# Kernel tuning notes

Hardware: AMD Instinct MI355X
Metric: run time of the kernel (lower is better)

## Reference

```python
import jax, jax.numpy as jnp
import numpy as np

N, E, K, F, R = 100000, 200000, 16, 32, 2
EPS = 1e-5

def setup_inputs() -> dict:
    key = jax.random.key(0)
    ks = jax.random.split(key, 32)
    inp = {}
    inp['x'] = jax.random.normal(ks[0], (N, F), jnp.float32)
    inp['y'] = jax.random.normal(ks[1], (E, F), jnp.float32)
    inp['deg_g'] = jax.random.uniform(ks[2], (N, 1), jnp.float32)
    inp['deg_lg'] = jax.random.uniform(ks[3], (E, 1), jnp.float32)
    inp['t_g'] = jax.random.randint(ks[4], (N, K), 0, N)
    inp['tt_g'] = jax.random.randint(ks[5], (N, K), 0, N)
    inp['t_lg'] = jax.random.randint(ks[6], (E, K), 0, E)
    inp['tt_lg'] = jax.random.randint(ks[7], (E, K), 0, E)
    inp['dst'] = jax.random.randint(ks[8], (E,), 0, N)
    inp['pm_pd'] = jax.random.randint(ks[9], (E,), 0, N)
    i = [10]
    def mk(shape):
        a = jax.random.normal(ks[i[0]], shape, jnp.float32) * 0.1
        i[0] += 1
        return a
    for nm in ['theta_x', 'theta_deg', 'theta_y', 'gamma_y', 'gamma_deg', 'gamma_x']:
        inp[nm + '_w'] = mk((F, F)); inp[nm + '_b'] = mk((F,))
    inp['theta_r_w'] = mk((R, F, F)); inp['theta_r_b'] = mk((R, F))
    inp['gamma_r_w'] = mk((R, F, F)); inp['gamma_r_b'] = mk((R, F))
    inp['bn_x_w'] = jnp.ones((F,), jnp.float32); inp['bn_x_b'] = jnp.zeros((F,), jnp.float32)
    inp['bn_y_w'] = jnp.ones((F,), jnp.float32); inp['bn_y_b'] = jnp.zeros((F,), jnp.float32)
    return inp

def _lin(a, w, b):
    return a @ w + b

def _bn(a, w, b):
    # BatchNorm1d in training mode: biased batch stats
    m = a.mean(axis=0)
    v = a.var(axis=0)
    return (a - m) / jnp.sqrt(v + EPS) * w + b

def _aggregate(z, t, tt):
    # per-node gather+sum over neighbor index lists (t: radius-0, tt: radius-1)
    return jnp.stack([z[t].sum(axis=1), z[tt].sum(axis=1)])  # [R, M, F]

def reference(x, y, deg_g, deg_lg, t_g, tt_g, t_lg, tt_lg, dst, pm_pd,
              theta_x_w, theta_x_b, theta_deg_w, theta_deg_b, theta_y_w, theta_y_b,
              gamma_y_w, gamma_y_b, gamma_deg_w, gamma_deg_b, gamma_x_w, gamma_x_b,
              theta_r_w, theta_r_b, gamma_r_w, gamma_r_b,
              bn_x_w, bn_x_b, bn_y_w, bn_y_b):
    n = F // 2
    pmpd_x = x[pm_pd]                                   # [E, F] embedding gather
    zs = _aggregate(x, t_g, tt_g)                        # [R, N, F]
    sum_x = jnp.einsum('rnf,rfo->no', zs, theta_r_w) + theta_r_b.sum(axis=0)
    pmpd_y = jax.ops.segment_sum(y, dst, num_segments=x.shape[0])  # copy_edge + sum
    xo = (_lin(x, theta_x_w, theta_x_b)
          + _lin(deg_g * x, theta_deg_w, theta_deg_b)
          + sum_x
          + _lin(pmpd_y, theta_y_w, theta_y_b))
    xo = jnp.concatenate([xo[:, :n], jax.nn.relu(xo[:, n:])], axis=1)
    xo = _bn(xo, bn_x_w, bn_x_b)
    zy = _aggregate(y, t_lg, tt_lg)                      # [R, E, F]
    sum_y = jnp.einsum('ref,rfo->eo', zy, gamma_r_w) + gamma_r_b.sum(axis=0)
    yo = (_lin(y, gamma_y_w, gamma_y_b)
          + _lin(deg_lg * y, gamma_deg_w, gamma_deg_b)
          + sum_y
          + _lin(pmpd_x, gamma_x_w, gamma_x_b))
    yo = jnp.concatenate([yo[:, :n], jax.nn.relu(yo[:, n:])], axis=1)
    yo = _bn(yo, bn_y_w, bn_y_b)
    return xo, yo
```

## Files before the change

kernel.cpp:

```cpp
#include <hip/hip_runtime.h>

#define NN 100000
#define NE 200000
#define MT (NN + NE)

typedef unsigned short u16;
typedef __attribute__((ext_vector_type(8))) short bf16x8;
typedef __attribute__((ext_vector_type(4))) float f32x4;

__device__ __forceinline__ float bf2f(u16 u) {
    union { unsigned int i; float f; } v; v.i = ((unsigned int)u) << 16; return v.f;
}
__device__ __forceinline__ u16 f2bf(float f) {
    union { unsigned int i; float f; } v; v.f = f;
    unsigned int r = v.i + 0x7fffu + ((v.i >> 16) & 1u);
    return (u16)(r >> 16);
}
__device__ __forceinline__ void unpack2(unsigned int u, float& lo, float& hi) {
    union { unsigned int i; float f; } a, b;
    a.i = u << 16; b.i = u & 0xffff0000u;
    lo = a.f; hi = b.f;
}
__device__ __forceinline__ unsigned int pack2(float a, float b) {
    return (unsigned int)f2bf(a) | ((unsigned int)f2bf(b) << 16);
}
__device__ __forceinline__ float loadf(const void* p, size_t i, int f32) {
    return f32 ? ((const float*)p)[i] : bf2f(((const u16*)p)[i]);
}
__device__ __forceinline__ void acc8(float a[8], uint4 g) {
    float e0, e1, e2, e3, e4, e5, e6, e7;
    unpack2(g.x, e0, e1); unpack2(g.y, e2, e3);
    unpack2(g.z, e4, e5); unpack2(g.w, e6, e7);
    a[0] += e0; a[1] += e1; a[2] += e2; a[3] += e3;
    a[4] += e4; a[5] += e5; a[6] += e6; a[7] += e7;
}

__global__ void detect_kernel(const unsigned int* __restrict__ x, int* flag) {
    __shared__ int cnt;
    if (threadIdx.x == 0) cnt = 0;
    __syncthreads();
    int bad = 0;
    for (int i = threadIdx.x; i < 1024; i += 256) {
        unsigned int e = (x[i] >> 7) & 0xFF;
        if (e == 0xFF || (e > 0 && (e < 107 || e > 134))) bad++;
    }
    atomicAdd(&cnt, bad);
    __syncthreads();
    if (threadIdx.x == 0) *flag = (cnt > 256) ? 1 : 0;
}

__global__ __launch_bounds__(256) void prep_kernel(
    const void* txw, const void* tdw, const void* tyw,
    const void* gyw, const void* gdw, const void* gxw,
    const void* trw, const void* grw,
    const void* txb, const void* tdb, const void* tyb,
    const void* gyb, const void* gdb, const void* gxb,
    const void* trb, const void* grb,
    u16* Bfx, u16* Bfy, float* bx, float* by, const int* flagp)
{
    int f32 = *flagp;
    int t = blockIdx.x * 256 + threadIdx.x;
    if (t < 4096) {
        int b = t >> 9, lane = (t >> 3) & 63, j = t & 7;
        int m = b >> 1;
        int k = ((lane >> 4) << 3) + j;
        int f = ((b & 1) << 4) + (lane & 15);
        size_t idx = (size_t)k * 32 + f;
        float v = (m == 0) ? loadf(txw, idx, f32) : (m == 1) ? loadf(tdw, idx, f32)
                : (m == 2) ? loadf(trw, idx, f32) : loadf(trw, 1024 + idx, f32);
        Bfx[t] = f2bf(v);
    } else if (t < 10240) {
        int e = t - 4096;
        int b = e >> 9, lane = (e >> 3) & 63, j = e & 7;
        int m = b >> 1;
        int k = ((lane >> 4) << 3) + j;
        int f = ((b & 1) << 4) + (lane & 15);
        size_t idx = (size_t)k * 32 + f;
        float v = (m == 0) ? loadf(gyw, idx, f32) : (m == 1) ? loadf(gdw, idx, f32)
                : (m == 2) ? loadf(grw, idx, f32) : (m == 3) ? loadf(grw, 1024 + idx, f32)
                : (m == 4) ? loadf(gxw, idx, f32) : loadf(tyw, idx, f32);
        Bfy[e] = f2bf(v);
    } else if (t < 10304) {
        int f = t - 10240;
        if (f < 32) {
            bx[f] = loadf(txb, f, f32) + loadf(tdb, f, f32) + loadf(tyb, f, f32)
                  + loadf(trb, f, f32) + loadf(trb, 32 + f, f32);
        } else {
            f -= 32;
            by[f] = loadf(gyb, f, f32) + loadf(gdb, f, f32) + loadf(gxb, f, f32)
                  + loadf(grb, f, f32) + loadf(grb, 32 + f, f32);
        }
    }
}

__global__ __launch_bounds__(256) void convert_kernel(
    const void* __restrict__ x, const void* __restrict__ y,
    u16* __restrict__ xb, u16* __restrict__ yb, const int* __restrict__ flagp)
{
    int f32 = *flagp;
    int t = blockIdx.x * 256 + threadIdx.x;
    if (t < NN * 4) {
        int r = t >> 2, q = t & 3;
        uint4 o;
        if (f32) {
            const float4* fp = (const float4*)((const float*)x + (size_t)r * 32 + q * 8);
            float4 v0 = fp[0], v1 = fp[1];
            o.x = pack2(v0.x, v0.y); o.y = pack2(v0.z, v0.w);
            o.z = pack2(v1.x, v1.y); o.w = pack2(v1.z, v1.w);
        } else {
            o = *(const uint4*)((const u16*)x + (size_t)r * 32 + q * 8);
        }
        *(uint4*)(xb + (size_t)r * 32 + q * 8) = o;
    } else if (t < MT * 4) {
        int t2 = t - NN * 4;
        int r = t2 >> 2, q = t2 & 3;
        uint4 o;
        if (f32) {
            const float4* fp = (const float4*)((const float*)y + (size_t)r * 32 + q * 8);
            float4 v0 = fp[0], v1 = fp[1];
            o.x = pack2(v0.x, v0.y); o.y = pack2(v0.z, v0.w);
            o.z = pack2(v1.x, v1.y); o.w = pack2(v1.z, v1.w);
        } else {
            o = *(const uint4*)((const u16*)y + (size_t)r * 32 + q * 8);
        }
        *(uint4*)(yb + (size_t)r * 32 + q * 8) = o;
    }
}

template<int IS_Y>
__global__ __launch_bounds__(256, 3) void fused_side(
    const u16* __restrict__ xb, const u16* __restrict__ yb,
    float* xacc,
    const u16* __restrict__ Bf, const float* __restrict__ bias,
    const void* __restrict__ deg,
    const int* __restrict__ tl, const int* __restrict__ ttl,
    const int* __restrict__ pm_pd, const int* __restrict__ dst,
    float* xpre, u16* __restrict__ ypre,
    float* __restrict__ stats, const int* __restrict__ flagp)
{
    __shared__ int s_t[1024];
    __shared__ int s_tt[1024];
    __shared__ float s_sum[32];
    __shared__ float s_sq[32];
    const int M = IS_Y ? NE : NN;
    int f32 = *flagp;
    int row0 = (int)blockIdx.x * 64;
    if (threadIdx.x < 32) { s_sum[threadIdx.x] = 0.f; s_sq[threadIdx.x] = 0.f; }
    int lim = (M - row0) * 16;
    for (int i = threadIdx.x; i < 1024; i += 256) {
        s_t[i]  = (i < lim) ? tl[(size_t)row0 * 16 + i]  : 0;
        s_tt[i] = (i < lim) ? ttl[(size_t)row0 * 16 + i] : 0;
    }
    __syncthreads();
    int lane = threadIdx.x & 63, wib = threadIdx.x >> 6;
    int r0 = row0 + wib * 16;
    if (r0 + 16 <= M) {
        const u16* tab = IS_Y ? yb : xb;
        int m = lane & 15, q = lane >> 4;
        int gr = r0 + m;
        const int* il  = &s_t[(wib * 16 + m) * 16];
        const int* ill = &s_tt[(wib * 16 + m) * 16];

        bf16x8 selfv = *(const bf16x8*)(tab + (size_t)gr * 32 + q * 8);
        union { u16 s[8]; bf16x8 v; } pm;
        if (IS_Y) {
            int ai = pm_pd[gr];
            pm.v = *(const bf16x8*)(xb + (size_t)ai * 32 + q * 8);
        }

        float aT[8]  = {0.f, 0.f, 0.f, 0.f, 0.f, 0.f, 0.f, 0.f};
        float aTT[8] = {0.f, 0.f, 0.f, 0.f, 0.f, 0.f, 0.f, 0.f};
        uint4 ga[8], gb[8];
#pragma unroll
        for (int j = 0; j < 8; ++j)
            ga[j] = *(const uint4*)(tab + (size_t)il[j] * 32 + q * 8);
#pragma unroll
        for (int j = 0; j < 8; ++j)
            gb[j] = *(const uint4*)(tab + (size_t)il[8 + j] * 32 + q * 8);
#pragma unroll
        for (int j = 0; j < 8; ++j) acc8(aT, ga[j]);
#pragma unroll
        for (int j = 0; j < 8; ++j)
            ga[j] = *(const uint4*)(tab + (size_t)ill[j] * 32 + q * 8);
#pragma unroll
        for (int j = 0; j < 8; ++j) acc8(aT, gb[j]);
#pragma unroll
        for (int j = 0; j < 8; ++j)
            gb[j] = *(const uint4*)(tab + (size_t)ill[8 + j] * 32 + q * 8);
#pragma unroll
        for (int j = 0; j < 8; ++j) acc8(aTT, ga[j]);
#pragma unroll
        for (int j = 0; j < 8; ++j) acc8(aTT, gb[j]);

        union { u16 s[8]; bf16x8 v; } ft, ftt;
#pragma unroll
        for (int j = 0; j < 8; ++j) { ft.s[j] = f2bf(aT[j]); ftt.s[j] = f2bf(aTT[j]); }

        const u16* bp = Bf + lane * 8;
#define BFR(b) (*(const bf16x8*)(bp + (b) * 512))
        f32x4 z = {0.f, 0.f, 0.f, 0.f};
        f32x4 a0, a1, d0, d1, c0 = z, c1 = z;
        a0 = __builtin_amdgcn_mfma_f32_16x16x32_bf16(selfv, BFR(0), z, 0, 0, 0);
        a1 = __builtin_amdgcn_mfma_f32_16x16x32_bf16(selfv, BFR(1), z, 0, 0, 0);
        d0 = __builtin_amdgcn_mfma_f32_16x16x32_bf16(selfv, BFR(2), z, 0, 0, 0);
        d1 = __builtin_amdgcn_mfma_f32_16x16x32_bf16(selfv, BFR(3), z, 0, 0, 0);
        a0 = __builtin_amdgcn_mfma_f32_16x16x32_bf16(ft.v,  BFR(4), a0, 0, 0, 0);
        a1 = __builtin_amdgcn_mfma_f32_16x16x32_bf16(ft.v,  BFR(5), a1, 0, 0, 0);
        a0 = __builtin_amdgcn_mfma_f32_16x16x32_bf16(ftt.v, BFR(6), a0, 0, 0, 0);
        a1 = __builtin_amdgcn_mfma_f32_16x16x32_bf16(ftt.v, BFR(7), a1, 0, 0, 0);
        if (IS_Y) {
            a0 = __builtin_amdgcn_mfma_f32_16x16x32_bf16(pm.v,  BFR(8),  a0, 0, 0, 0);
            a1 = __builtin_amdgcn_mfma_f32_16x16x32_bf16(pm.v,  BFR(9),  a1, 0, 0, 0);
            c0 = __builtin_amdgcn_mfma_f32_16x16x32_bf16(selfv, BFR(10), z, 0, 0, 0);
            c1 = __builtin_amdgcn_mfma_f32_16x16x32_bf16(selfv, BFR(11), z, 0, 0, 0);
        }
#undef BFR

        int n = m;
        int rowb = r0 + q * 4;
        float bl_ = bias[n], bh_ = bias[16 + n];
        float s0 = 0.f, q0 = 0.f, s1 = 0.f, q1 = 0.f;
#pragma unroll
        for (int i = 0; i < 4; ++i) {
            float dgi = loadf(deg, rowb + i, f32);
            size_t ro = (size_t)(rowb + i) * 32;
            float lo = a0[i] + dgi * d0[i] + bl_;
            float hi = a1[i] + dgi * d1[i] + bh_;
            if (!IS_Y) {
                lo += xacc[ro + n];
                hi += xacc[ro + 16 + n];
            }
            hi = fmaxf(hi, 0.f);
            if (!IS_Y) {
                xpre[ro + n]      = lo;
                xpre[ro + 16 + n] = hi;
            } else {
                ypre[ro + n]      = f2bf(lo);
                ypre[ro + 16 + n] = f2bf(hi);
                int d = dst[rowb + i];
                float* p = xacc + (size_t)d * 32;
                atomicAdd(p + n,      c0[i]);
                atomicAdd(p + 16 + n, c1[i]);
            }
            s0 += lo; q0 += lo * lo;
            s1 += hi; q1 += hi * hi;
        }
        atomicAdd(&s_sum[n], s0);      atomicAdd(&s_sq[n], q0);
        atomicAdd(&s_sum[16 + n], s1); atomicAdd(&s_sq[16 + n], q1);
    }
    __syncthreads();
    if (threadIdx.x < 32) {
        float* ss = stats + (IS_Y ? 64 : 0);
        atomicAdd(&ss[threadIdx.x], s_sum[threadIdx.x]);
        atomicAdd(&ss[32 + threadIdx.x], s_sq[threadIdx.x]);
    }
}

__global__ void finalize_stats(
    const float* stats,
    const void* bnxw, const void* bnxb, const void* bnyw, const void* bnyb,
    float* scsh, const int* flagp)
{
    int f32 = *flagp;
    int f = threadIdx.x;
    if (f < 32) {
        float m = stats[f] / (float)NN;
        float var = stats[32 + f] / (float)NN - m * m;
        float inv = rsqrtf(var + 1e-5f);
        float sc = loadf(bnxw, f, f32) * inv;
        scsh[f] = sc; scsh[32 + f] = loadf(bnxb, f, f32) - m * sc;
    } else if (f < 64) {
        int g = f - 32;
        float m = stats[64 + g] / (float)NE;
        float var = stats[96 + g] / (float)NE - m * m;
        float inv = rsqrtf(var + 1e-5f);
        float sc = loadf(bnyw, g, f32) * inv;
        scsh[64 + g] = sc; scsh[96 + g] = loadf(bnyb, g, f32) - m * sc;
    }
}

__global__ __launch_bounds__(256) void apply_bn(
    const float* __restrict__ xpre, const u16* __restrict__ ypre,
    const float* __restrict__ scsh, void* __restrict__ out,
    const int* __restrict__ flagp)
{
    int f32 = *flagp;
    int tid = blockIdx.x * 256 + threadIdx.x;
    if (tid >= MT * 8) return;
    int fq = (tid & 7) * 4;
    const float* sc;
    float4 v;
    if (tid < NN * 8) {
        v = ((const float4*)xpre)[tid];
        sc = scsh;
    } else {
        size_t off = (size_t)tid * 4 - (size_t)NN * 32;
        ushort4 u = *(const ushort4*)(ypre + off);
        v.x = bf2f(u.x); v.y = bf2f(u.y); v.z = bf2f(u.z); v.w = bf2f(u.w);
        sc = scsh + 64;
    }
    float o0 = v.x * sc[fq + 0] + sc[32 + fq + 0];
    float o1 = v.y * sc[fq + 1] + sc[32 + fq + 1];
    float o2 = v.z * sc[fq + 2] + sc[32 + fq + 2];
    float o3 = v.w * sc[fq + 3] + sc[32 + fq + 3];
    if (f32) {
        float4 o; o.x = o0; o.y = o1; o.z = o2; o.w = o3;
        ((float4*)out)[tid] = o;
    } else {
        ushort4 o; o.x = f2bf(o0); o.y = f2bf(o1); o.z = f2bf(o2); o.w = f2bf(o3);
        ((ushort4*)out)[tid] = o;
    }
}

extern "C" void kernel_launch(void* const* d_in, const int* in_sizes, int n_in,
                              void* d_out, int out_size, void* d_ws, size_t ws_size,
                              hipStream_t stream)
{
    const void* x      = d_in[0];
    const void* y      = d_in[1];
    const void* deg_g  = d_in[2];
    const void* deg_lg = d_in[3];
    const int* t_g   = (const int*)d_in[4];
    const int* tt_g  = (const int*)d_in[5];
    const int* t_lg  = (const int*)d_in[6];
    const int* tt_lg = (const int*)d_in[7];
    const int* dst   = (const int*)d_in[8];
    const int* pm_pd = (const int*)d_in[9];

    char* ws = (char*)d_ws;
    int*   flag = (int*)ws;
    u16* Bfx   = (u16*)(ws + 256);
    u16* Bfy   = Bfx + 4096;
    float* bx  = (float*)(ws + 24576);
    float* by  = bx + 32;
    float* stats = by + 32;
    float* scsh  = stats + 128;
    u16* xb    = (u16*)(ws + 65536);
    u16* yb    = xb + (size_t)NN * 32;
    float* xacc = (float*)(yb + (size_t)NE * 32);
    u16* ypre  = (u16*)(xacc + (size_t)NN * 32);

    hipMemsetAsync(stats, 0, 256 * sizeof(float), stream);
    hipMemsetAsync(xacc, 0, (size_t)NN * 32 * sizeof(float), stream);

    detect_kernel<<<1, 256, 0, stream>>>((const unsigned int*)x, flag);
    prep_kernel<<<41, 256, 0, stream>>>(
        d_in[10], d_in[12], d_in[14], d_in[16], d_in[18], d_in[20],
        d_in[22], d_in[24],
        d_in[11], d_in[13], d_in[15], d_in[17], d_in[19], d_in[21],
        d_in[23], d_in[25],
        Bfx, Bfy, bx, by, flag);
    convert_kernel<<<4688, 256, 0, stream>>>(x, y, xb, yb, flag);
    fused_side<1><<<3125, 256, 0, stream>>>(xb, yb, xacc, Bfy, by, deg_lg,
                                            t_lg, tt_lg, pm_pd, dst,
                                            (float*)0, ypre, stats, flag);
    fused_side<0><<<1563, 256, 0, stream>>>(xb, yb, xacc, Bfx, bx, deg_g,
                                            t_g, tt_g, pm_pd, dst,
                                            xacc , (u16*)0,
                                            stats, flag);
    finalize_stats<<<1, 64, 0, stream>>>(stats, d_in[26], d_in[27], d_in[28],
                                         d_in[29], scsh, flag);
    apply_bn<<<9375, 256, 0, stream>>>(xacc, ypre, scsh, d_out, flag);
}
```

Baseline: 405.5 us.

## Merge x and y side kernels into one interleaved launch with separate x-stats pass

```diff
diff --git a/kernel.cpp b/kernel.cpp
--- a/kernel.cpp
+++ b/kernel.cpp
@@ -128,28 +128,25 @@
 }
 
 template<int IS_Y>
-__global__ __launch_bounds__(256, 3) void fused_side(
+__device__ __forceinline__ void fused_body(
     const u16* __restrict__ xb, const u16* __restrict__ yb,
     float* xacc,
     const u16* __restrict__ Bf, const float* __restrict__ bias,
     const void* __restrict__ deg,
     const int* __restrict__ tl, const int* __restrict__ ttl,
     const int* __restrict__ pm_pd, const int* __restrict__ dst,
-    float* xpre, u16* __restrict__ ypre,
-    float* __restrict__ stats, const int* __restrict__ flagp)
-{
-    __shared__ int s_t[1024];
-    __shared__ int s_tt[1024];
-    __shared__ float s_sum[32];
-    __shared__ float s_sq[32];
+    float* __restrict__ xmfma, u16* __restrict__ ypre,
+    float* __restrict__ ystats, int f32, int sb,
+    int* s_t, int* s_tt, float* s_sum, float* s_sq)
+{
     const int M = IS_Y ? NE : NN;
-    int f32 = *flagp;
-    int row0 = (int)blockIdx.x * 64;
-    if (threadIdx.x < 32) { s_sum[threadIdx.x] = 0.f; s_sq[threadIdx.x] = 0.f; }
+    int row0 = sb * 64;
+    if (row0 >= M) return;
+    if (IS_Y && threadIdx.x < 32) { s_sum[threadIdx.x] = 0.f; s_sq[threadIdx.x] = 0.f; }
     int lim = (M - row0) * 16;
     for (int i = threadIdx.x; i < 1024; i += 256) {
-        s_t[i]  = (i < lim) ? tl[(size_t)row0 * 16 + i]  : 0;
-        s_tt[i] = (i < lim) ? ttl[(size_t)row0 * 16 + i] : 0;
+        s_t[i]  = (i < lim) ? __builtin_nontemporal_load(&tl[(size_t)row0 * 16 + i])  : 0;
+        s_tt[i] = (i < lim) ? __builtin_nontemporal_load(&ttl[(size_t)row0 * 16 + i]) : 0;
     }
     __syncthreads();
     int lane = threadIdx.x & 63, wib = threadIdx.x >> 6;
@@ -227,32 +224,90 @@
             float lo = a0[i] + dgi * d0[i] + bl_;
             float hi = a1[i] + dgi * d1[i] + bh_;
             if (!IS_Y) {
-                lo += xacc[ro + n];
-                hi += xacc[ro + 16 + n];
-            }
-            hi = fmaxf(hi, 0.f);
-            if (!IS_Y) {
-                xpre[ro + n]      = lo;
-                xpre[ro + 16 + n] = hi;
+                __builtin_nontemporal_store(lo, &xmfma[ro + n]);
+                __builtin_nontemporal_store(hi, &xmfma[ro + 16 + n]);
             } else {
-                ypre[ro + n]      = f2bf(lo);
-                ypre[ro + 16 + n] = f2bf(hi);
+                hi = fmaxf(hi, 0.f);
+                __builtin_nontemporal_store(f2bf(lo), &ypre[ro + n]);
+                __builtin_nontemporal_store(f2bf(hi), &ypre[ro + 16 + n]);
                 int d = dst[rowb + i];
                 float* p = xacc + (size_t)d * 32;
                 atomicAdd(p + n,      c0[i]);
                 atomicAdd(p + 16 + n, c1[i]);
+                s0 += lo; q0 += lo * lo;
+                s1 += hi; q1 += hi * hi;
             }
-            s0 += lo; q0 += lo * lo;
-            s1 += hi; q1 += hi * hi;
-        }
-        atomicAdd(&s_sum[n], s0);      atomicAdd(&s_sq[n], q0);
-        atomicAdd(&s_sum[16 + n], s1); atomicAdd(&s_sq[16 + n], q1);
-    }
+        }
+        if (IS_Y) {
+            atomicAdd(&s_sum[n], s0);      atomicAdd(&s_sq[n], q0);
+            atomicAdd(&s_sum[16 + n], s1); atomicAdd(&s_sq[16 + n], q1);
+        }
+    }
+    if (IS_Y) {
+        __syncthreads();
+        if (threadIdx.x < 32) {
+            atomicAdd(&ystats[threadIdx.x], s_sum[threadIdx.x]);
+            atomicAdd(&ystats[32 + threadIdx.x], s_sq[threadIdx.x]);
+        }
+    }
+}
+
+__global__ __launch_bounds__(256, 3) void fused_both(
+    const u16* __restrict__ xb, const u16* __restrict__ yb, float* xacc,
+    const u16* __restrict__ Bfx, const u16* __restrict__ Bfy,
+    const float* __restrict__ bx, const float* __restrict__ by,
+    const void* __restrict__ deg_g, const void* __restrict__ deg_lg,
+    const int* __restrict__ t_g, const int* __restrict__ tt_g,
+    const int* __restrict__ t_lg, const int* __restrict__ tt_lg,
+    const int* __restrict__ pm_pd, const int* __restrict__ dst,
+    float* __restrict__ xmfma, u16* __restrict__ ypre,
+    float* __restrict__ stats, const int* __restrict__ flagp)
+{
+    __shared__ int s_t[1024];
+    __shared__ int s_tt[1024];
+    __shared__ float s_sum[32];
+    __shared__ float s_sq[32];
+    int f32 = *flagp;
+    int bid = blockIdx.x;
+    int s = bid % 3;
+    if (s == 2) {
+        fused_body<0>(xb, yb, xacc, Bfx, bx, deg_g, t_g, tt_g, pm_pd, dst,
+                      xmfma, ypre, stats, f32, bid / 3,
+                      s_t, s_tt, s_sum, s_sq);
+    } else {
+        fused_body<1>(xb, yb, xacc, Bfy, by, deg_lg, t_lg, tt_lg, pm_pd, dst,
+                      xmfma, ypre, stats + 64, f32, (bid / 3) * 2 + s,
+                      s_t, s_tt, s_sum, s_sq);
+    }
+}
+
+__global__ __launch_bounds__(256) void xstats_kernel(
+    const float* __restrict__ xmfma, float* __restrict__ xacc,
+    float* __restrict__ stats)
+{
+    __shared__ float s_sum[32];
+    __shared__ float s_sq[32];
+    if (threadIdx.x < 32) { s_sum[threadIdx.x] = 0.f; s_sq[threadIdx.x] = 0.f; }
+    __syncthreads();
+    int tid = blockIdx.x * 256 + threadIdx.x;
+    int fq = (tid & 7) * 4;
+    float4 a = ((const float4*)xmfma)[tid];
+    float4 b = ((const float4*)xacc)[tid];
+    float v0 = a.x + b.x, v1 = a.y + b.y, v2 = a.z + b.z, v3 = a.w + b.w;
+    if (fq >= 16) {
+        v0 = fmaxf(v0, 0.f); v1 = fmaxf(v1, 0.f);
+        v2 = fmaxf(v2, 0.f); v3 = fmaxf(v3, 0.f);
+    }
+    float4 o; o.x = v0; o.y = v1; o.z = v2; o.w = v3;
+    ((float4*)xacc)[tid] = o;
+    atomicAdd(&s_sum[fq + 0], v0); atomicAdd(&s_sq[fq + 0], v0 * v0);
+    atomicAdd(&s_sum[fq + 1], v1); atomicAdd(&s_sq[fq + 1], v1 * v1);
+    atomicAdd(&s_sum[fq + 2], v2); atomicAdd(&s_sq[fq + 2], v2 * v2);
+    atomicAdd(&s_sum[fq + 3], v3); atomicAdd(&s_sq[fq + 3], v3 * v3);
     __syncthreads();
     if (threadIdx.x < 32) {
-        float* ss = stats + (IS_Y ? 64 : 0);
-        atomicAdd(&ss[threadIdx.x], s_sum[threadIdx.x]);
-        atomicAdd(&ss[32 + threadIdx.x], s_sq[threadIdx.x]);
+        atomicAdd(&stats[threadIdx.x], s_sum[threadIdx.x]);
+        atomicAdd(&stats[32 + threadIdx.x], s_sq[threadIdx.x]);
     }
 }
 
@@ -339,6 +394,7 @@
     u16* yb    = xb + (size_t)NN * 32;
     float* xacc = (float*)(yb + (size_t)NE * 32);
     u16* ypre  = (u16*)(xacc + (size_t)NN * 32);
+    float* xmfma = (float*)(ypre + (size_t)NE * 32);
 
     hipMemsetAsync(stats, 0, 256 * sizeof(float), stream);
     hipMemsetAsync(xacc, 0, (size_t)NN * 32 * sizeof(float), stream);
@@ -351,13 +407,10 @@
         d_in[23], d_in[25],
         Bfx, Bfy, bx, by, flag);
     convert_kernel<<<4688, 256, 0, stream>>>(x, y, xb, yb, flag);
-    fused_side<1><<<3125, 256, 0, stream>>>(xb, yb, xacc, Bfy, by, deg_lg,
-                                            t_lg, tt_lg, pm_pd, dst,
-                                            (float*)0, ypre, stats, flag);
-    fused_side<0><<<1563, 256, 0, stream>>>(xb, yb, xacc, Bfx, bx, deg_g,
-                                            t_g, tt_g, pm_pd, dst,
-                                            xacc , (u16*)0,
-                                            stats, flag);
+    fused_both<<<4689, 256, 0, stream>>>(xb, yb, xacc, Bfx, Bfy, bx, by,
+                                         deg_g, deg_lg, t_g, tt_g, t_lg, tt_lg,
+                                         pm_pd, dst, xmfma, ypre, stats, flag);
+    xstats_kernel<<<3125, 256, 0, stream>>>(xmfma, xacc, stats);
     finalize_stats<<<1, 64, 0, stream>>>(stats, d_in[26], d_in[27], d_in[28],
                                          d_in[29], scsh, flag);
     apply_bn<<<9375, 256, 0, stream>>>(xacc, ypre, scsh, d_out, flag);
```

After: 450.0 us. +11.0%, slower.
